# Optimization experiments

Hardware: AMD Instinct MI355X
Metric: run time of the kernel (lower is better)

The kernel has to match this reference:

```python
import jax, jax.numpy as jnp
import numpy as np

EPS = 1e-6
B, T, D, A = 16, 2048, 512, 128
SCALE = A ** (-0.5)


def _xavier(key, fan_in, fan_out):
    limit = np.sqrt(6.0 / (fan_in + fan_out)).astype(np.float32)
    return jax.random.uniform(key, (fan_in, fan_out), jnp.float32, -limit, limit)


def setup_inputs() -> dict:
    key = jax.random.key(0)
    kx, kq, kk, kv = jax.random.split(key, 4)
    x = jax.random.normal(kx, (B, T, D), jnp.float32)
    Wq = _xavier(kq, D, A)
    Wk = _xavier(kk, D, A)
    Wv = _xavier(kv, D, 1)
    bq = jnp.full((A,), 0.01, jnp.float32)
    bk = jnp.full((A,), 0.01, jnp.float32)
    bv = jnp.full((1,), 0.01, jnp.float32)
    return {"x": x, "Wq": Wq, "bq": bq, "Wk": Wk, "bk": bk, "Wv": Wv, "bv": bv}


def reference(x, Wq, bq, Wk, bk, Wv, bv):
    # mean-variance norm over features (torch.std default is unbiased -> ddof=1)
    mu = jnp.mean(x, axis=-1, keepdims=True)
    sd = jnp.std(x, axis=-1, keepdims=True, ddof=1)
    xn = (x - mu) / (sd + EPS)
    Q = xn @ Wq + bq            # [B, T, A]
    K = xn @ Wk + bk            # [B, T, A]
    V = xn @ Wv + bv            # [B, T, 1]
    scores = jnp.einsum("bta,bsa->bts", Q, K) * SCALE  # [B, T, T]
    w_att = jax.nn.softmax(scores, axis=-1)
    w = jnp.einsum("bts,bso->bto", w_att, V)           # [B, T, 1]
    return (w, w_att)
```

## Files before the change

### kernel.cpp

```cpp
#include <hip/hip_runtime.h>

#define NB 16
#define NT 2048
#define ND 512
#define NA 128
#define EPSV 1e-6f
#define SCALE 0.08838834764831845f
#define NCH 4
#define SCH 512

typedef __bf16 bf16;
typedef __bf16 bf16x4 __attribute__((ext_vector_type(4)));
typedef __bf16 bf16x8 __attribute__((ext_vector_type(8)));
typedef float f32x4 __attribute__((ext_vector_type(4)));

__global__ void prep_wt(const float* __restrict__ Wq, const float* __restrict__ Wk,
                        bf16* __restrict__ WT) {
    int n = blockIdx.x;
    const float* W = (n < NA) ? Wq : Wk;
    int col = n & (NA - 1);
    for (int k = threadIdx.x; k < ND; k += blockDim.x)
        WT[(size_t)n * ND + k] = (bf16)W[(size_t)k * NA + col];
}

__launch_bounds__(256)
__global__ void norm_proj(const float* __restrict__ x, const float* __restrict__ Wv,
                          const float* __restrict__ bvp, const bf16* __restrict__ WT,
                          const float* __restrict__ bq, const float* __restrict__ bk,
                          bf16* __restrict__ Qm, bf16* __restrict__ Km,
                          float* __restrict__ Vout) {
    __shared__ bf16 xn[16 * ND];
    const int tid = threadIdx.x;
    const int lane = tid & 63, wv = tid >> 6;
    const int row0 = blockIdx.x * 16;

    float wvv[8];
    float sumw = 0.f;
#pragma unroll
    for (int i = 0; i < 4; ++i) { wvv[i]     = Wv[lane * 4 + i];       sumw += wvv[i]; }
#pragma unroll
    for (int i = 0; i < 4; ++i) { wvv[4 + i] = Wv[256 + lane * 4 + i]; sumw += wvv[4 + i]; }
#pragma unroll
    for (int m = 1; m < 64; m <<= 1) sumw += __shfl_xor(sumw, m);
    const float bvs = bvp[0];

#pragma unroll
    for (int r = 0; r < 4; ++r) {
        const int lrow = wv * 4 + r;
        const int grow = row0 + lrow;
        const float* xr = x + (size_t)grow * ND;
        f32x4 a = *(const f32x4*)(xr + lane * 4);
        f32x4 b = *(const f32x4*)(xr + 256 + lane * 4);
        float s = 0.f, sq = 0.f, dw = 0.f;
#pragma unroll
        for (int i = 0; i < 4; ++i) { s += a[i]; sq += a[i] * a[i]; dw += a[i] * wvv[i]; }
#pragma unroll
        for (int i = 0; i < 4; ++i) { s += b[i]; sq += b[i] * b[i]; dw += b[i] * wvv[4 + i]; }
#pragma unroll
        for (int m = 1; m < 64; m <<= 1) {
            s  += __shfl_xor(s, m);
            sq += __shfl_xor(sq, m);
            dw += __shfl_xor(dw, m);
        }
        const float mu  = s * (1.f / 512.f);
        float var = (sq - 512.f * mu * mu) * (1.f / 511.f);
        var = fmaxf(var, 0.f);
        const float inv = 1.f / (sqrtf(var) + EPSV);
        if (lane == 0) Vout[grow] = (dw - mu * sumw) * inv + bvs;

        const int sw = (lrow & 7) << 4;
        bf16x4 v0, v1;
#pragma unroll
        for (int i = 0; i < 4; ++i) v0[i] = (bf16)((a[i] - mu) * inv);
#pragma unroll
        for (int i = 0; i < 4; ++i) v1[i] = (bf16)((b[i] - mu) * inv);
        *(bf16x4*)((char*)xn + lrow * 1024 + ((lane * 8) ^ sw))       = v0;
        *(bf16x4*)((char*)xn + lrow * 1024 + ((512 + lane * 8) ^ sw)) = v1;
    }
    __syncthreads();

    const int c = lane & 15, g = lane >> 4;
    const int asw = (c & 7) << 4;
    f32x4 acc[4];
#pragma unroll
    for (int i = 0; i < 4; ++i) acc[i] = f32x4{0.f, 0.f, 0.f, 0.f};

    for (int ks = 0; ks < 16; ++ks) {
        const bf16x8 af = *(const bf16x8*)((const char*)xn + c * 1024 +
                                           ((ks * 64 + g * 16) ^ asw));
#pragma unroll
        for (int i = 0; i < 4; ++i) {
            const int n = wv * 64 + i * 16 + c;
            const bf16x8 bfr = *(const bf16x8*)(WT + (size_t)n * ND + ks * 32 + g * 8);
            acc[i] = __builtin_amdgcn_mfma_f32_16x16x32_bf16(af, bfr, acc[i], 0, 0, 0);
        }
    }
#pragma unroll
    for (int i = 0; i < 4; ++i) {
        const int n = wv * 64 + i * 16 + c;
        const float bias = (n < NA) ? bq[n] : bk[n - NA];
        bf16* dst = (n < NA) ? (Qm + n) : (Km + (n - NA));
#pragma unroll
        for (int j = 0; j < 4; ++j)
            dst[(size_t)(row0 + g * 4 + j) * NA] = (bf16)(acc[i][j] + bias);
    }
}

__launch_bounds__(256)
__global__ void attn_pass1(const bf16* __restrict__ Qm, const bf16* __restrict__ Km,
                           const float* __restrict__ Vg,
                           float* __restrict__ pl, float* __restrict__ pw) {
    __shared__ bf16 Kt[64 * NA];
    const int tid = threadIdx.x;
    const int lane = tid & 63, wv = tid >> 6;
    const int b = blockIdx.z, t0 = blockIdx.x * 64, sc = blockIdx.y;
    const int c = lane & 15, g = lane >> 4;
    const int trow = t0 + wv * 16 + c;

    bf16x8 qf[4];
    const bf16* qrow = Qm + (size_t)(b * NT + trow) * NA;
#pragma unroll
    for (int ks = 0; ks < 4; ++ks) qf[ks] = *(const bf16x8*)(qrow + ks * 32 + g * 8);

    const int srow = tid >> 4, scc = tid & 15;
    const bf16* kbase = Km + (size_t)(b * NT + sc * SCH + srow) * NA + scc * 8;
    bf16* kdst = (bf16*)((char*)Kt + srow * 256 + ((scc * 16) ^ ((srow & 7) << 4)));
    bf16x8 sreg[4];

#pragma unroll
    for (int i = 0; i < 4; ++i)
        sreg[i] = *(const bf16x8*)(kbase + (size_t)(i * 16) * NA);
#pragma unroll
    for (int i = 0; i < 4; ++i)
        *(bf16x8*)((char*)kdst + i * 16 * 256) = sreg[i];
    __syncthreads();

    const float* vbase = Vg + b * NT + sc * SCH;
    float l_loc = 0.f, w_loc = 0.f;

    for (int tt = 0; tt < SCH / 64; ++tt) {
        if (tt + 1 < SCH / 64) {
#pragma unroll
            for (int i = 0; i < 4; ++i)
                sreg[i] = *(const bf16x8*)(kbase + (size_t)((tt + 1) * 64 + i * 16) * NA);
        }

#pragma unroll
        for (int ns = 0; ns < 4; ++ns) {
            f32x4 acc = f32x4{0.f, 0.f, 0.f, 0.f};
            const int rr = ns * 16 + c;
            const int rsw = (rr & 7) << 4;
#pragma unroll
            for (int ks = 0; ks < 4; ++ks) {
                const bf16x8 afr = *(const bf16x8*)((const char*)Kt + rr * 256 +
                                                    ((ks * 64 + g * 16) ^ rsw));
                acc = __builtin_amdgcn_mfma_f32_16x16x32_bf16(afr, qf[ks], acc, 0, 0, 0);
            }
            const f32x4 vv = *(const f32x4*)(vbase + tt * 64 + ns * 16 + g * 4);
#pragma unroll
            for (int jj = 0; jj < 4; ++jj) {
                const float p = __expf(acc[jj] * SCALE);
                l_loc += p;
                w_loc += p * vv[jj];
            }
        }

        if (tt + 1 < SCH / 64) {
            __syncthreads();
#pragma unroll
            for (int i = 0; i < 4; ++i)
                *(bf16x8*)((char*)kdst + i * 16 * 256) = sreg[i];
            __syncthreads();
        }
    }

#pragma unroll
    for (int mask = 16; mask <= 32; mask <<= 1) {
        l_loc += __shfl_xor(l_loc, mask);
        w_loc += __shfl_xor(w_loc, mask);
    }
    if (g == 0) {
        const int idx = sc * (NB * NT) + b * NT + trow;
        pl[idx] = l_loc;
        pw[idx] = w_loc;
    }
}

__global__ void attn_reduce(const float* __restrict__ pl, const float* __restrict__ pw,
                            float* __restrict__ linv, float* __restrict__ out_w) {
    const int r = blockIdx.x * 256 + threadIdx.x;
    float L = 0.f, W = 0.f;
#pragma unroll
    for (int ch = 0; ch < NCH; ++ch) {
        L += pl[ch * (NB * NT) + r];
        W += pw[ch * (NB * NT) + r];
    }
    linv[r] = 1.f / L;
    out_w[r] = W / L;
}

__launch_bounds__(256)
__global__ void attn_pass2(const bf16* __restrict__ Qm, const bf16* __restrict__ Km,
                           const float* __restrict__ linv, float* __restrict__ out_att) {
    __shared__ bf16 Kt[64 * NA];
    const int tid = threadIdx.x;
    const int lane = tid & 63, wv = tid >> 6;
    const int b = blockIdx.z, t0 = blockIdx.x * 64, sc = blockIdx.y;
    const int c = lane & 15, g = lane >> 4;
    const int trow = t0 + wv * 16 + c;

    bf16x8 qf[4];
    const bf16* qrow = Qm + (size_t)(b * NT + trow) * NA;
#pragma unroll
    for (int ks = 0; ks < 4; ++ks) qf[ks] = *(const bf16x8*)(qrow + ks * 32 + g * 8);

    const float lrow = linv[b * NT + trow];
    float* orow = out_att + (size_t)(b * NT + trow) * NT;

    const int srow = tid >> 4, scc = tid & 15;
    const bf16* kbase = Km + (size_t)(b * NT + sc * SCH + srow) * NA + scc * 8;
    bf16* kdst = (bf16*)((char*)Kt + srow * 256 + ((scc * 16) ^ ((srow & 7) << 4)));
    bf16x8 sreg[4];

#pragma unroll
    for (int i = 0; i < 4; ++i)
        sreg[i] = *(const bf16x8*)(kbase + (size_t)(i * 16) * NA);
#pragma unroll
    for (int i = 0; i < 4; ++i)
        *(bf16x8*)((char*)kdst + i * 16 * 256) = sreg[i];
    __syncthreads();

    for (int tt = 0; tt < SCH / 64; ++tt) {
        if (tt + 1 < SCH / 64) {
#pragma unroll
            for (int i = 0; i < 4; ++i)
                sreg[i] = *(const bf16x8*)(kbase + (size_t)((tt + 1) * 64 + i * 16) * NA);
        }

        const int s0 = sc * SCH + tt * 64;
#pragma unroll
        for (int ns = 0; ns < 4; ++ns) {
            f32x4 acc = f32x4{0.f, 0.f, 0.f, 0.f};
            const int rr = ns * 16 + c;
            const int rsw = (rr & 7) << 4;
#pragma unroll
            for (int ks = 0; ks < 4; ++ks) {
                const bf16x8 afr = *(const bf16x8*)((const char*)Kt + rr * 256 +
                                                    ((ks * 64 + g * 16) ^ rsw));
                acc = __builtin_amdgcn_mfma_f32_16x16x32_bf16(afr, qf[ks], acc, 0, 0, 0);
            }
            f32x4 w;
#pragma unroll
            for (int jj = 0; jj < 4; ++jj)
                w[jj] = __expf(acc[jj] * SCALE) * lrow;
            *(f32x4*)(orow + s0 + ns * 16 + g * 4) = w;
        }

        if (tt + 1 < SCH / 64) {
            __syncthreads();
#pragma unroll
            for (int i = 0; i < 4; ++i)
                *(bf16x8*)((char*)kdst + i * 16 * 256) = sreg[i];
            __syncthreads();
        }
    }
}

extern "C" void kernel_launch(void* const* d_in, const int* in_sizes, int n_in,
                              void* d_out, int out_size, void* d_ws, size_t ws_size,
                              hipStream_t stream) {
    const float* x  = (const float*)d_in[0];
    const float* Wq = (const float*)d_in[1];
    const float* bq = (const float*)d_in[2];
    const float* Wk = (const float*)d_in[3];
    const float* bk = (const float*)d_in[4];
    const float* Wv = (const float*)d_in[5];
    const float* bv = (const float*)d_in[6];

    float* out_w   = (float*)d_out;
    float* out_att = (float*)d_out + NB * NT;

    char* ws = (char*)d_ws;
    bf16*  WT   = (bf16*)ws;
    float* V    = (float*)(ws + 262144);
    bf16*  Qm   = (bf16*)(ws + 393216);
    bf16*  Km   = (bf16*)(ws + 393216 + 8388608);
    float* pl   = (float*)(ws + 17170432);
    float* pw   = (float*)(ws + 17694720);
    float* linv = (float*)(ws + 18219008);

    prep_wt<<<dim3(256), dim3(256), 0, stream>>>(Wq, Wk, WT);
    norm_proj<<<dim3((NB * NT) / 16), dim3(256), 0, stream>>>(x, Wv, bv, WT, bq, bk, Qm, Km, V);
    attn_pass1<<<dim3(NT / 64, NCH, NB), dim3(256), 0, stream>>>(Qm, Km, V, pl, pw);
    attn_reduce<<<dim3((NB * NT) / 256), dim3(256), 0, stream>>>(pl, pw, linv, out_w);
    attn_pass2<<<dim3(NT / 64, NCH, NB), dim3(256), 0, stream>>>(Qm, Km, linv, out_att);
}
```

Before: 176.6 us.

## Keep whole K chunk resident in LDS and loop query tiles per block

Attention passes now load a 128-row K chunk into shared memory once and iterate over 512 query rows per block, replacing the streamed 64-row K tiles with per-step barriers. The grid shrinks to fewer, longer blocks with a 4-blocks-per-CU launch bound. The partial sum/weight buffers are placed in the attention output region as scratch, since pass2 overwrites it afterward. This trades parallelism and more LDS per block for reduced K reloads and synchronization.

Measured after the change: 289.4 us. +63.9%, slower.

```diff
diff --git a/kernel.cpp b/kernel.cpp
--- a/kernel.cpp
+++ b/kernel.cpp
@@ -6,8 +6,9 @@
 #define NA 128
 #define EPSV 1e-6f
 #define SCALE 0.08838834764831845f
-#define NCH 4
-#define SCH 512
+#define NCH 16
+#define SCH 128
+#define NTSL 4
 
 typedef __bf16 bf16;
 typedef __bf16 bf16x4 __attribute__((ext_vector_type(4)));
@@ -106,47 +107,40 @@
     }
 }
 
-__launch_bounds__(256)
+__launch_bounds__(256, 4)
 __global__ void attn_pass1(const bf16* __restrict__ Qm, const bf16* __restrict__ Km,
                            const float* __restrict__ Vg,
                            float* __restrict__ pl, float* __restrict__ pw) {
-    __shared__ bf16 Kt[64 * NA];
+    __shared__ bf16 Kt[SCH * NA];
     const int tid = threadIdx.x;
     const int lane = tid & 63, wv = tid >> 6;
-    const int b = blockIdx.z, t0 = blockIdx.x * 64, sc = blockIdx.y;
+    const int tsl = blockIdx.x, sc = blockIdx.y, b = blockIdx.z;
     const int c = lane & 15, g = lane >> 4;
-    const int trow = t0 + wv * 16 + c;
-
-    bf16x8 qf[4];
-    const bf16* qrow = Qm + (size_t)(b * NT + trow) * NA;
-#pragma unroll
-    for (int ks = 0; ks < 4; ++ks) qf[ks] = *(const bf16x8*)(qrow + ks * 32 + g * 8);
-
-    const int srow = tid >> 4, scc = tid & 15;
-    const bf16* kbase = Km + (size_t)(b * NT + sc * SCH + srow) * NA + scc * 8;
-    bf16* kdst = (bf16*)((char*)Kt + srow * 256 + ((scc * 16) ^ ((srow & 7) << 4)));
-    bf16x8 sreg[4];
-
-#pragma unroll
-    for (int i = 0; i < 4; ++i)
-        sreg[i] = *(const bf16x8*)(kbase + (size_t)(i * 16) * NA);
-#pragma unroll
-    for (int i = 0; i < 4; ++i)
-        *(bf16x8*)((char*)kdst + i * 16 * 256) = sreg[i];
+
+    {
+        const int srow = tid >> 4, scc = tid & 15;
+        const bf16* kbase = Km + (size_t)(b * NT + sc * SCH + srow) * NA + scc * 8;
+        char* kdst = (char*)Kt + srow * 256 + ((scc * 16) ^ ((srow & 7) << 4));
+#pragma unroll
+        for (int i = 0; i < 8; ++i) {
+            const bf16x8 v = *(const bf16x8*)(kbase + (size_t)(i * 16) * NA);
+            *(bf16x8*)(kdst + i * 16 * 256) = v;
+        }
+    }
     __syncthreads();
 
     const float* vbase = Vg + b * NT + sc * SCH;
-    float l_loc = 0.f, w_loc = 0.f;
-
-    for (int tt = 0; tt < SCH / 64; ++tt) {
-        if (tt + 1 < SCH / 64) {
-#pragma unroll
-            for (int i = 0; i < 4; ++i)
-                sreg[i] = *(const bf16x8*)(kbase + (size_t)((tt + 1) * 64 + i * 16) * NA);
-        }
-
-#pragma unroll
-        for (int ns = 0; ns < 4; ++ns) {
+
+    for (int ti = 0; ti < 8; ++ti) {
+        const int trow = tsl * 512 + ti * 64 + wv * 16 + c;
+        const bf16* qrow = Qm + (size_t)(b * NT + trow) * NA;
+        bf16x8 qf[4];
+#pragma unroll
+        for (int ks = 0; ks < 4; ++ks) qf[ks] = *(const bf16x8*)(qrow + ks * 32 + g * 8);
+
+        float l_loc = 0.f, w_loc = 0.f;
+#pragma unroll
+        for (int ns = 0; ns < 8; ++ns) {
             f32x4 acc = f32x4{0.f, 0.f, 0.f, 0.f};
             const int rr = ns * 16 + c;
             const int rsw = (rr & 7) << 4;
@@ -156,7 +150,7 @@
                                                     ((ks * 64 + g * 16) ^ rsw));
                 acc = __builtin_amdgcn_mfma_f32_16x16x32_bf16(afr, qf[ks], acc, 0, 0, 0);
             }
-            const f32x4 vv = *(const f32x4*)(vbase + tt * 64 + ns * 16 + g * 4);
+            const f32x4 vv = *(const f32x4*)(vbase + ns * 16 + g * 4);
 #pragma unroll
             for (int jj = 0; jj < 4; ++jj) {
                 const float p = __expf(acc[jj] * SCALE);
@@ -164,25 +158,16 @@
                 w_loc += p * vv[jj];
             }
         }
-
-        if (tt + 1 < SCH / 64) {
-            __syncthreads();
-#pragma unroll
-            for (int i = 0; i < 4; ++i)
-                *(bf16x8*)((char*)kdst + i * 16 * 256) = sreg[i];
-            __syncthreads();
-        }
-    }
-
-#pragma unroll
-    for (int mask = 16; mask <= 32; mask <<= 1) {
-        l_loc += __shfl_xor(l_loc, mask);
-        w_loc += __shfl_xor(w_loc, mask);
-    }
-    if (g == 0) {
-        const int idx = sc * (NB * NT) + b * NT + trow;
-        pl[idx] = l_loc;
-        pw[idx] = w_loc;
+#pragma unroll
+        for (int mask = 16; mask <= 32; mask <<= 1) {
+            l_loc += __shfl_xor(l_loc, mask);
+            w_loc += __shfl_xor(w_loc, mask);
+        }
+        if (g == 0) {
+            const int idx = sc * (NB * NT) + b * NT + trow;
+            pl[idx] = l_loc;
+            pw[idx] = w_loc;
+        }
     }
 }
 
@@ -199,47 +184,38 @@
     out_w[r] = W / L;
 }
 
-__launch_bounds__(256)
+__launch_bounds__(256, 4)
 __global__ void attn_pass2(const bf16* __restrict__ Qm, const bf16* __restrict__ Km,
                            const float* __restrict__ linv, float* __restrict__ out_att) {
-    __shared__ bf16 Kt[64 * NA];
+    __shared__ bf16 Kt[SCH * NA];
     const int tid = threadIdx.x;
     const int lane = tid & 63, wv = tid >> 6;
-    const int b = blockIdx.z, t0 = blockIdx.x * 64, sc = blockIdx.y;
+    const int tsl = blockIdx.x, sc = blockIdx.y, b = blockIdx.z;
     const int c = lane & 15, g = lane >> 4;
-    const int trow = t0 + wv * 16 + c;
-
-    bf16x8 qf[4];
-    const bf16* qrow = Qm + (size_t)(b * NT + trow) * NA;
-#pragma unroll
-    for (int ks = 0; ks < 4; ++ks) qf[ks] = *(const bf16x8*)(qrow + ks * 32 + g * 8);
-
-    const float lrow = linv[b * NT + trow];
-    float* orow = out_att + (size_t)(b * NT + trow) * NT;
-
-    const int srow = tid >> 4, scc = tid & 15;
-    const bf16* kbase = Km + (size_t)(b * NT + sc * SCH + srow) * NA + scc * 8;
-    bf16* kdst = (bf16*)((char*)Kt + srow * 256 + ((scc * 16) ^ ((srow & 7) << 4)));
-    bf16x8 sreg[4];
-
-#pragma unroll
-    for (int i = 0; i < 4; ++i)
-        sreg[i] = *(const bf16x8*)(kbase + (size_t)(i * 16) * NA);
-#pragma unroll
-    for (int i = 0; i < 4; ++i)
-        *(bf16x8*)((char*)kdst + i * 16 * 256) = sreg[i];
+
+    {
+        const int srow = tid >> 4, scc = tid & 15;
+        const bf16* kbase = Km + (size_t)(b * NT + sc * SCH + srow) * NA + scc * 8;
+        char* kdst = (char*)Kt + srow * 256 + ((scc * 16) ^ ((srow & 7) << 4));
+#pragma unroll
+        for (int i = 0; i < 8; ++i) {
+            const bf16x8 v = *(const bf16x8*)(kbase + (size_t)(i * 16) * NA);
+            *(bf16x8*)(kdst + i * 16 * 256) = v;
+        }
+    }
     __syncthreads();
 
-    for (int tt = 0; tt < SCH / 64; ++tt) {
-        if (tt + 1 < SCH / 64) {
-#pragma unroll
-            for (int i = 0; i < 4; ++i)
-                sreg[i] = *(const bf16x8*)(kbase + (size_t)((tt + 1) * 64 + i * 16) * NA);
-        }
-
-        const int s0 = sc * SCH + tt * 64;
-#pragma unroll
-        for (int ns = 0; ns < 4; ++ns) {
+    for (int ti = 0; ti < 8; ++ti) {
+        const int trow = tsl * 512 + ti * 64 + wv * 16 + c;
+        const bf16* qrow = Qm + (size_t)(b * NT + trow) * NA;
+        bf16x8 qf[4];
+#pragma unroll
+        for (int ks = 0; ks < 4; ++ks) qf[ks] = *(const bf16x8*)(qrow + ks * 32 + g * 8);
+        const float lrow = linv[b * NT + trow];
+        float* orow = out_att + (size_t)(b * NT + trow) * NT + sc * SCH;
+
+#pragma unroll
+        for (int ns = 0; ns < 8; ++ns) {
             f32x4 acc = f32x4{0.f, 0.f, 0.f, 0.f};
             const int rr = ns * 16 + c;
             const int rsw = (rr & 7) << 4;
@@ -253,15 +229,7 @@
 #pragma unroll
             for (int jj = 0; jj < 4; ++jj)
                 w[jj] = __expf(acc[jj] * SCALE) * lrow;
-            *(f32x4*)(orow + s0 + ns * 16 + g * 4) = w;
-        }
-
-        if (tt + 1 < SCH / 64) {
-            __syncthreads();
-#pragma unroll
-            for (int i = 0; i < 4; ++i)
-                *(bf16x8*)((char*)kdst + i * 16 * 256) = sreg[i];
-            __syncthreads();
+            *(f32x4*)(orow + ns * 16 + g * 4) = w;
         }
     }
 }
@@ -285,13 +253,14 @@
     float* V    = (float*)(ws + 262144);
     bf16*  Qm   = (bf16*)(ws + 393216);
     bf16*  Km   = (bf16*)(ws + 393216 + 8388608);
-    float* pl   = (float*)(ws + 17170432);
-    float* pw   = (float*)(ws + 17694720);
-    float* linv = (float*)(ws + 18219008);
+    float* linv = (float*)(ws + 17170432);
+
+    float* pl = out_att;
+    float* pw = out_att + NCH * (NB * NT);
 
     prep_wt<<<dim3(256), dim3(256), 0, stream>>>(Wq, Wk, WT);
     norm_proj<<<dim3((NB * NT) / 16), dim3(256), 0, stream>>>(x, Wv, bv, WT, bq, bk, Qm, Km, V);
-    attn_pass1<<<dim3(NT / 64, NCH, NB), dim3(256), 0, stream>>>(Qm, Km, V, pl, pw);
+    attn_pass1<<<dim3(NTSL, NCH, NB), dim3(256), 0, stream>>>(Qm, Km, V, pl, pw);
     attn_reduce<<<dim3((NB * NT) / 256), dim3(256), 0, stream>>>(pl, pw, linv, out_w);
-    attn_pass2<<<dim3(NT / 64, NCH, NB), dim3(256), 0, stream>>>(Qm, Km, linv, out_att);
-}
+    attn_pass2<<<dim3(NTSL, NCH, NB), dim3(256), 0, stream>>>(Qm, Km, linv, out_att);
+}
```
